# Performance work log

Measured on AMD Instinct MI355X. Metric: run time of the kernel, lower is better.

## Reference

```python
import jax, jax.numpy as jnp
import numpy as np

GROUPS = 8

def conv1d(x, w, b, stride=1, groups=1):
    # x: [B,C,L], w: [O, I//groups, K]
    y = jax.lax.conv_general_dilated(x, w, (stride,), 'VALID',
        dimension_numbers=('NCH', 'OIH', 'NCH'), feature_group_count=groups)
    return y + b[None, :, None]

def shuffle1d(x, groups):
    B, C, L = x.shape
    cpg = C // groups
    return x.reshape(B, groups, cpg, L).transpose(0, 2, 1, 3).reshape(B, C, L)

def setup_inputs() -> dict:
    key = jax.random.key(0)
    ks = jax.random.split(key, 12)
    C = 256
    B, L = 8, 4096
    g = GROUPS
    sc = 0.05
    inp = {
        'x':   jax.random.normal(ks[0], (B, C, L), dtype=jnp.float32),
        'w1':  jax.random.normal(ks[1], (C, C // g, 3), dtype=jnp.float32) * sc,
        'b1':  jax.random.normal(ks[2], (C,), dtype=jnp.float32) * sc,
        'w2':  jax.random.normal(ks[3], (C, C // g, 3), dtype=jnp.float32) * sc,
        'b2':  jax.random.normal(ks[4], (C,), dtype=jnp.float32) * sc,
        'wa1': jax.random.normal(ks[5], (C, 2 * C // g, 1), dtype=jnp.float32) * sc,
        'ba1': jax.random.normal(ks[6], (C,), dtype=jnp.float32) * sc,
        'wa2': jax.random.normal(ks[7], (C, C // g, 1), dtype=jnp.float32) * sc,
        'ba2': jax.random.normal(ks[8], (C,), dtype=jnp.float32) * sc,
        'w3':  jax.random.normal(ks[9], (C, C // g, 5), dtype=jnp.float32) * sc,  # kernel_size-4=5
        'b3':  jax.random.normal(ks[10], (C,), dtype=jnp.float32) * sc,
    }
    return inp

def reference(x, w1, b1, w2, b2, wa1, ba1, wa2, ba2, w3, b3):
    g = GROUPS
    # in_state has length 0 at init, so cat is identity; L >= kernel_size.
    h = conv1d(x, w1, b1, stride=1, groups=g)      # [B,C,L-2]
    h = shuffle1d(h, g)
    h = conv1d(h, w2, b2, stride=1, groups=g)      # [B,C,L-4]
    h = shuffle1d(h, g)
    # SortAttn: stable ascending sort over channel dim
    sorted_h = jnp.sort(h, axis=1, stable=True)
    a = conv1d(jnp.concatenate((sorted_h, h), axis=1), wa1, ba1, stride=1, groups=g)
    a = shuffle1d(a, g)
    a = jax.nn.sigmoid(conv1d(a, wa2, ba2, stride=1, groups=g))
    h = h * a
    y = conv1d(h, w3, b3, stride=1, groups=g)      # [B,C,L-8]
    return y
```

## Files before the change

### kernel.cpp

```cpp
#include <hip/hip_runtime.h>
#include <math.h>

#define BB 8
#define CCH 256
#define LLEN 4096
#define L1V 4094
#define L2V 4092
#define L3V 4088
#define NCOL (BB * L2V)

__global__ void prep_kernel(const float* __restrict__ wa1, const float* __restrict__ wa2,
                            const float* __restrict__ w1, const float* __restrict__ w2,
                            const float* __restrict__ w3,
                            float* __restrict__ wt1T, float* __restrict__ wt2T,
                            float* __restrict__ w1T, float* __restrict__ w2T,
                            float* __restrict__ w3T) {
    int r = blockIdx.x;
    int o = threadIdx.x;
    if (r < 64) {
        wt1T[r * 256 + o] = wa1[o * 64 + r];
    } else if (r < 96) {
        wt2T[(r - 64) * 256 + o] = wa2[o * 32 + (r - 64)];
    } else if (r < 192) {
        w1T[(r - 96) * 256 + o] = w1[o * 96 + (r - 96)];
    } else if (r < 288) {
        w2T[(r - 192) * 256 + o] = w2[o * 96 + (r - 192)];
    } else {
        w3T[(r - 288) * 256 + o] = w3[o * 160 + (r - 288)];
    }
}

__global__ __launch_bounds__(256, 4) void conv1_kernel(const float* __restrict__ x,
                                                       const float* __restrict__ w1T,
                                                       const float* __restrict__ b1,
                                                       float* __restrict__ t1) {
    __shared__ float xs[9248];
    const int b = blockIdx.y;
    const int l0 = blockIdx.x * 32;
    const int t = threadIdx.x;

#pragma unroll
    for (int j = 0; j < 9; ++j) {
        int f = t + 256 * j;
        int row = f / 9;
        int q = f - row * 9;
        size_t rb = (size_t)(b * CCH + row) * LLEN;
        float4 v;
        int base = l0 + 4 * q;
        if (base + 3 < LLEN) {
            v = *(const float4*)(x + rb + base);
        } else {
            v.x = x[rb + min(base + 0, LLEN - 1)];
            v.y = x[rb + min(base + 1, LLEN - 1)];
            v.z = x[rb + min(base + 2, LLEN - 1)];
            v.w = x[rb + min(base + 3, LLEN - 1)];
        }
        int a = row * 36 + (row >> 5) * 4 + 4 * q;
        *(float4*)&xs[a] = v;
    }
    __syncthreads();

    const int oc = t;
    const int go = t >> 5;
    float acc[32];
#pragma unroll
    for (int l = 0; l < 32; ++l) acc[l] = 0.f;

    for (int i = 0; i < 32; ++i) {
        int row = go * 32 + i;
        int base = row * 36 + go * 4;
        float wv0 = w1T[(i * 3 + 0) * 256 + oc];
        float wv1 = w1T[(i * 3 + 1) * 256 + oc];
        float wv2 = w1T[(i * 3 + 2) * 256 + oc];
#pragma unroll
        for (int q = 0; q < 9; ++q) {
            float4 v = *(const float4*)&xs[base + 4 * q];
#pragma unroll
            for (int j = 0; j < 4; ++j) {
                int e = 4 * q + j;
                float xv = (&v.x)[j];
                if (e < 32) acc[e] += wv0 * xv;
                if (e >= 1 && e <= 32) acc[e - 1] += wv1 * xv;
                if (e >= 2 && e <= 33) acc[e - 2] += wv2 * xv;
            }
        }
    }
    float bias = b1[oc];
    int nc = (oc & 31) * 8 + (oc >> 5);
    float* dst = t1 + (size_t)(b * L1V + l0) * CCH + nc;
#pragma unroll
    for (int l = 0; l < 32; ++l) {
        if (l0 + l < L1V) dst[(size_t)l * CCH] = acc[l] + bias;
    }
}

__global__ __launch_bounds__(256, 4) void conv2_kernel(const float* __restrict__ t1,
                                                       const float* __restrict__ w2T,
                                                       const float* __restrict__ b2,
                                                       float* __restrict__ t2) {
    __shared__ float ts[9792];
    const int b = blockIdx.y;
    const int l0 = blockIdx.x * 32;
    const int t = threadIdx.x;

#pragma unroll
    for (int j = 0; j < 9; ++j) {
        int f = t + 256 * j;
        if (f < 2176) {
            int p = f >> 6;
            int c4 = (f & 63) * 4;
            int row = min(l0 + p, L1V - 1);
            float4 v = *(const float4*)(t1 + (size_t)(b * L1V + row) * CCH + c4);
            *(float4*)&ts[p * 288 + (c4 >> 5) * 36 + (c4 & 31)] = v;
        }
    }
    __syncthreads();

    const int oc = t;
    const int go = t >> 5;
    float acc[32];
#pragma unroll
    for (int l = 0; l < 32; ++l) acc[l] = 0.f;

    for (int i4 = 0; i4 < 8; ++i4) {
        float wv[12];
#pragma unroll
        for (int z = 0; z < 12; ++z) wv[z] = w2T[(i4 * 12 + z) * 256 + oc];
        int colbase = go * 36 + i4 * 4;
#pragma unroll
        for (int p = 0; p < 34; ++p) {
            float4 rv = *(const float4*)&ts[p * 288 + colbase];
#pragma unroll
            for (int cc = 0; cc < 4; ++cc) {
                float xv = (&rv.x)[cc];
#pragma unroll
                for (int k = 0; k < 3; ++k) {
                    int l = p - k;
                    if (l >= 0 && l < 32) acc[l] += wv[cc * 3 + k] * xv;
                }
            }
        }
    }
    float bias = b2[oc];
    int nc = (oc & 31) * 8 + (oc >> 5);
    float* dst = t2 + (size_t)(b * L2V + l0) * CCH + nc;
#pragma unroll
    for (int l = 0; l < 32; ++l) {
        if (l0 + l < L2V) dst[(size_t)l * CCH] = acc[l] + bias;
    }
}

__device__ __forceinline__ void ce_pair(float& a, float& b, bool up) {
    float lo = fminf(a, b), hi = fmaxf(a, b);
    a = up ? lo : hi;
    b = up ? hi : lo;
}

template<int LM>
__device__ __forceinline__ float swz(float x) {
    return __int_as_float(__builtin_amdgcn_ds_swizzle(__float_as_int(x), (LM << 10) | 0x1F));
}

template<int K, int J>
__device__ __forceinline__ void mstep(float v[4][4], int lane) {
    if constexpr (J >= 4) {
        constexpr int LM = J >> 2;
        const bool upper = (lane & LM) != 0;
#pragma unroll
        for (int r = 0; r < 4; ++r) {
            const bool dirUp = (((4 * lane + r) & K) == 0);
            const bool keepMin = (dirUp != upper);
#pragma unroll
            for (int c = 0; c < 4; ++c) {
                float other;
                if constexpr (LM == 32) other = __shfl_xor(v[c][r], 32, 64);
                else other = swz<LM>(v[c][r]);
                float lo = fminf(v[c][r], other), hi = fmaxf(v[c][r], other);
                v[c][r] = keepMin ? lo : hi;
            }
        }
    } else if constexpr (J == 2) {
#pragma unroll
        for (int r = 0; r < 2; ++r) {
            const bool up = (((4 * lane + r) & K) == 0);
#pragma unroll
            for (int c = 0; c < 4; ++c) ce_pair(v[c][r], v[c][r + 2], up);
        }
    } else {
#pragma unroll
        for (int r = 0; r < 4; r += 2) {
            const bool up = (((4 * lane + r) & K) == 0);
#pragma unroll
            for (int c = 0; c < 4; ++c) ce_pair(v[c][r], v[c][r + 1], up);
        }
    }
    if constexpr (J > 1) mstep<K, (J >> 1)>(v, lane);
}

template<int K>
__device__ __forceinline__ void msort(float v[4][4], int lane) {
    mstep<K, (K >> 1)>(v, lane);
    if constexpr (K < 256) msort<(K << 1)>(v, lane);
}

__global__ __launch_bounds__(256, 5) void attn_kernel(float* __restrict__ t2,
                                                      const float* __restrict__ wt1T,
                                                      const float* __restrict__ wt2T,
                                                      const float* __restrict__ ba1,
                                                      const float* __restrict__ ba2) {
    __shared__ float sm[8192];
    const int t = threadIdx.x;
    const int wv = t >> 6;
    const int lane = t & 63;
    const int wbase = wv << 11;
    const int go = lane >> 3;

    float4 ba1v = *(const float4*)&ba1[4 * lane];
    float4 ba2v = *(const float4*)&ba2[4 * lane];

    const int colBase = blockIdx.x * 16 + wv * 4;

    float4 hv[4];
#pragma unroll
    for (int cc = 0; cc < 4; ++cc) {
        hv[cc] = *(const float4*)(t2 + (size_t)(colBase + cc) * CCH + 4 * lane);
    }
#pragma unroll
    for (int r = 0; r < 4; ++r) {
        int e = 4 * lane + r;
        int ch = (e >> 6) + 4;
        int slot = ch * 64 + ((e & 63) ^ ch);
        float4 vvv = make_float4((&hv[0].x)[r], (&hv[1].x)[r], (&hv[2].x)[r], (&hv[3].x)[r]);
        *(float4*)&sm[wbase + slot * 4] = vvv;
    }
    float v[4][4];
#pragma unroll
    for (int cc = 0; cc < 4; ++cc)
#pragma unroll
        for (int r = 0; r < 4; ++r) v[cc][r] = (&hv[cc].x)[r];
    msort<2>(v, lane);

#pragma unroll
    for (int r = 0; r < 4; ++r) {
        int e = 4 * lane + r;
        int ch = e >> 6;
        int slot = ch * 64 + ((e & 63) ^ ch);
        float4 vvv = make_float4(v[0][r], v[1][r], v[2][r], v[3][r]);
        *(float4*)&sm[wbase + slot * 4] = vvv;
    }

    float4 acc[4];
#pragma unroll
    for (int cc = 0; cc < 4; ++cc) acc[cc] = make_float4(0.f, 0.f, 0.f, 0.f);
#pragma unroll 4
    for (int i = 0; i < 64; ++i) {
        float4 w4 = *(const float4*)&wt1T[i * 256 + 4 * lane];
        float4 cv = *(const float4*)&sm[wbase + (go * 64 + (i ^ go)) * 4];
#pragma unroll
        for (int cc = 0; cc < 4; ++cc) {
            float cvv = (&cv.x)[cc];
            acc[cc].x += w4.x * cvv;
            acc[cc].y += w4.y * cvv;
            acc[cc].z += w4.z * cvv;
            acc[cc].w += w4.w * cvv;
        }
    }
#pragma unroll
    for (int r = 0; r < 4; ++r) {
        float bb = (&ba1v.x)[r];
        float4 vvv = make_float4((&acc[0].x)[r] + bb, (&acc[1].x)[r] + bb,
                                 (&acc[2].x)[r] + bb, (&acc[3].x)[r] + bb);
        *(float4*)&sm[wbase + (5 * lane + r) * 4] = vvv;
    }

    float4 acc2[4];
#pragma unroll
    for (int cc = 0; cc < 4; ++cc) acc2[cc] = make_float4(0.f, 0.f, 0.f, 0.f);
#pragma unroll 4
    for (int i = 0; i < 32; ++i) {
        float4 w4 = *(const float4*)&wt2T[i * 256 + 4 * lane];
        int idx = ((i & 7) << 5) + (go << 2) + (i >> 3);
        int slotA = idx + (idx >> 2);
        float4 av = *(const float4*)&sm[wbase + slotA * 4];
#pragma unroll
        for (int cc = 0; cc < 4; ++cc) {
            float avv = (&av.x)[cc];
            acc2[cc].x += w4.x * avv;
            acc2[cc].y += w4.y * avv;
            acc2[cc].z += w4.z * avv;
            acc2[cc].w += w4.w * avv;
        }
    }
#pragma unroll
    for (int cc = 0; cc < 4; ++cc) {
        float zx = acc2[cc].x + ba2v.x;
        float zy = acc2[cc].y + ba2v.y;
        float zz = acc2[cc].z + ba2v.z;
        float zw = acc2[cc].w + ba2v.w;
        float4 res;
        res.x = hv[cc].x * (1.f / (1.f + __expf(-zx)));
        res.y = hv[cc].y * (1.f / (1.f + __expf(-zy)));
        res.z = hv[cc].z * (1.f / (1.f + __expf(-zz)));
        res.w = hv[cc].w * (1.f / (1.f + __expf(-zw)));
        *(float4*)(t2 + (size_t)(colBase + cc) * CCH + 4 * lane) = res;
    }
}

__global__ __launch_bounds__(256, 4) void conv3_kernel(const float* __restrict__ hm,
                                                       const float* __restrict__ w3T,
                                                       const float* __restrict__ b3,
                                                       float* __restrict__ out) {
    __shared__ float ts[9216];
    const int b = blockIdx.y;
    const int l0 = blockIdx.x * 32;
    const int t = threadIdx.x;

#pragma unroll
    for (int j = 0; j < 9; ++j) {
        int f = t + 256 * j;
        int p = f >> 6;
        int c4 = (f & 63) * 4;
        int row = min(l0 + p, L2V - 1);
        float4 v = *(const float4*)(hm + (size_t)(b * L2V + row) * CCH + c4);
        *(float4*)&ts[p * 256 + c4] = v;
    }
    __syncthreads();

    const int oc = t;
    const int go = t >> 5;
    float acc[32];
#pragma unroll
    for (int l = 0; l < 32; ++l) acc[l] = 0.f;

    for (int i4 = 0; i4 < 8; ++i4) {
        float wv[20];
#pragma unroll
        for (int z = 0; z < 20; ++z) wv[z] = w3T[(i4 * 20 + z) * 256 + oc];
        int colbase = go * 32 + i4 * 4;
#pragma unroll
        for (int p = 0; p < 36; ++p) {
            float4 rv = *(const float4*)&ts[p * 256 + colbase];
#pragma unroll
            for (int cc = 0; cc < 4; ++cc) {
                float xv = (&rv.x)[cc];
#pragma unroll
                for (int k = 0; k < 5; ++k) {
                    int l = p - k;
                    if (l >= 0 && l < 32) acc[l] += wv[cc * 5 + k] * xv;
                }
            }
        }
    }
    float bias = b3[oc];
    float* dst = out + (size_t)(b * CCH + oc) * L3V + l0;
#pragma unroll
    for (int l4 = 0; l4 < 8; ++l4) {
        int gl = l0 + 4 * l4;
        if (gl + 3 < L3V) {
            float4 v;
            v.x = acc[4 * l4 + 0] + bias;
            v.y = acc[4 * l4 + 1] + bias;
            v.z = acc[4 * l4 + 2] + bias;
            v.w = acc[4 * l4 + 3] + bias;
            *(float4*)(dst + 4 * l4) = v;
        } else {
#pragma unroll
            for (int c = 0; c < 4; ++c) {
                if (gl + c < L3V) dst[4 * l4 + c] = acc[4 * l4 + c] + bias;
            }
        }
    }
}

extern "C" void kernel_launch(void* const* d_in, const int* in_sizes, int n_in,
                              void* d_out, int out_size, void* d_ws, size_t ws_size,
                              hipStream_t stream) {
    const float* x   = (const float*)d_in[0];
    const float* w1  = (const float*)d_in[1];
    const float* b1  = (const float*)d_in[2];
    const float* w2  = (const float*)d_in[3];
    const float* b2  = (const float*)d_in[4];
    const float* wa1 = (const float*)d_in[5];
    const float* ba1 = (const float*)d_in[6];
    const float* wa2 = (const float*)d_in[7];
    const float* ba2 = (const float*)d_in[8];
    const float* w3  = (const float*)d_in[9];
    const float* b3  = (const float*)d_in[10];
    float* out = (float*)d_out;

    char* ws = (char*)d_ws;
    float* t1   = (float*)ws;
    float* t2   = (float*)(ws + ((size_t)32 << 20));
    float* wt1T = (float*)(ws + ((size_t)64 << 20));
    float* wt2T = wt1T + 64 * 256;
    float* w1T  = wt2T + 32 * 256;
    float* w2T  = w1T + 96 * 256;
    float* w3T  = w2T + 96 * 256;

    hipLaunchKernelGGL(prep_kernel, dim3(448), dim3(256), 0, stream,
                       wa1, wa2, w1, w2, w3, wt1T, wt2T, w1T, w2T, w3T);
    hipLaunchKernelGGL(conv1_kernel, dim3(128, BB), dim3(256), 0, stream, x, w1T, b1, t1);
    hipLaunchKernelGGL(conv2_kernel, dim3(128, BB), dim3(256), 0, stream, t1, w2T, b2, t2);
    hipLaunchKernelGGL(attn_kernel, dim3(2046), dim3(256), 0, stream, t2, wt1T, wt2T, ba1, ba2);
    hipLaunchKernelGGL(conv3_kernel, dim3(128, BB), dim3(256), 0, stream, t2, w3T, b3, out);
}
```

Before: 284.5 us.

## Fuse conv1 and conv2 into one kernel with halo recompute in shared memory

Merges the first two grouped convolutions into a single kernel. Each block computes 34 conv1 output positions (a 2-column halo), writes them with the channel shuffle applied into shared memory, and then runs conv2 directly from shared memory. This removes the t1 global write and read round trip and one kernel launch. The cost is a small amount of recomputed halo work, 34 live accumulators instead of 32 (more register pressure), and an extra sync.

```diff
diff --git a/kernel.cpp b/kernel.cpp
--- a/kernel.cpp
+++ b/kernel.cpp
@@ -30,11 +30,13 @@
     }
 }
 
-__global__ __launch_bounds__(256, 4) void conv1_kernel(const float* __restrict__ x,
-                                                       const float* __restrict__ w1T,
-                                                       const float* __restrict__ b1,
-                                                       float* __restrict__ t1) {
-    __shared__ float xs[9248];
+__global__ __launch_bounds__(256, 4) void conv12_kernel(const float* __restrict__ x,
+                                                        const float* __restrict__ w1T,
+                                                        const float* __restrict__ b1,
+                                                        const float* __restrict__ w2T,
+                                                        const float* __restrict__ b2,
+                                                        float* __restrict__ t2) {
+    __shared__ float sm[9792];
     const int b = blockIdx.y;
     const int l0 = blockIdx.x * 32;
     const int t = threadIdx.x;
@@ -56,15 +58,16 @@
             v.w = x[rb + min(base + 3, LLEN - 1)];
         }
         int a = row * 36 + (row >> 5) * 4 + 4 * q;
-        *(float4*)&xs[a] = v;
+        *(float4*)&sm[a] = v;
     }
     __syncthreads();
 
     const int oc = t;
     const int go = t >> 5;
-    float acc[32];
-#pragma unroll
-    for (int l = 0; l < 32; ++l) acc[l] = 0.f;
+
+    float acc[34];
+#pragma unroll
+    for (int l = 0; l < 34; ++l) acc[l] = 0.f;
 
     for (int i = 0; i < 32; ++i) {
         int row = go * 32 + i;
@@ -74,53 +77,29 @@
         float wv2 = w1T[(i * 3 + 2) * 256 + oc];
 #pragma unroll
         for (int q = 0; q < 9; ++q) {
-            float4 v = *(const float4*)&xs[base + 4 * q];
+            float4 v = *(const float4*)&sm[base + 4 * q];
 #pragma unroll
             for (int j = 0; j < 4; ++j) {
                 int e = 4 * q + j;
                 float xv = (&v.x)[j];
-                if (e < 32) acc[e] += wv0 * xv;
-                if (e >= 1 && e <= 32) acc[e - 1] += wv1 * xv;
-                if (e >= 2 && e <= 33) acc[e - 2] += wv2 * xv;
-            }
-        }
-    }
-    float bias = b1[oc];
-    int nc = (oc & 31) * 8 + (oc >> 5);
-    float* dst = t1 + (size_t)(b * L1V + l0) * CCH + nc;
-#pragma unroll
-    for (int l = 0; l < 32; ++l) {
-        if (l0 + l < L1V) dst[(size_t)l * CCH] = acc[l] + bias;
-    }
-}
-
-__global__ __launch_bounds__(256, 4) void conv2_kernel(const float* __restrict__ t1,
-                                                       const float* __restrict__ w2T,
-                                                       const float* __restrict__ b2,
-                                                       float* __restrict__ t2) {
-    __shared__ float ts[9792];
-    const int b = blockIdx.y;
-    const int l0 = blockIdx.x * 32;
-    const int t = threadIdx.x;
-
-#pragma unroll
-    for (int j = 0; j < 9; ++j) {
-        int f = t + 256 * j;
-        if (f < 2176) {
-            int p = f >> 6;
-            int c4 = (f & 63) * 4;
-            int row = min(l0 + p, L1V - 1);
-            float4 v = *(const float4*)(t1 + (size_t)(b * L1V + row) * CCH + c4);
-            *(float4*)&ts[p * 288 + (c4 >> 5) * 36 + (c4 & 31)] = v;
-        }
-    }
+                if (e < 34) acc[e] += wv0 * xv;
+                if (e >= 1 && e <= 34) acc[e - 1] += wv1 * xv;
+                if (e >= 2) acc[e - 2] += wv2 * xv;
+            }
+        }
+    }
+    float bias1 = b1[oc];
+    int c1 = (oc & 31) * 8 + (oc >> 5);
+    int col1 = (c1 >> 5) * 36 + (c1 & 31);
+
     __syncthreads();
-
-    const int oc = t;
-    const int go = t >> 5;
-    float acc[32];
-#pragma unroll
-    for (int l = 0; l < 32; ++l) acc[l] = 0.f;
+#pragma unroll
+    for (int p = 0; p < 34; ++p) sm[p * 288 + col1] = acc[p] + bias1;
+    __syncthreads();
+
+    float acc2[32];
+#pragma unroll
+    for (int l = 0; l < 32; ++l) acc2[l] = 0.f;
 
     for (int i4 = 0; i4 < 8; ++i4) {
         float wv[12];
@@ -129,24 +108,24 @@
         int colbase = go * 36 + i4 * 4;
 #pragma unroll
         for (int p = 0; p < 34; ++p) {
-            float4 rv = *(const float4*)&ts[p * 288 + colbase];
+            float4 rv = *(const float4*)&sm[p * 288 + colbase];
 #pragma unroll
             for (int cc = 0; cc < 4; ++cc) {
                 float xv = (&rv.x)[cc];
 #pragma unroll
                 for (int k = 0; k < 3; ++k) {
                     int l = p - k;
-                    if (l >= 0 && l < 32) acc[l] += wv[cc * 3 + k] * xv;
+                    if (l >= 0 && l < 32) acc2[l] += wv[cc * 3 + k] * xv;
                 }
             }
         }
     }
-    float bias = b2[oc];
+    float bias2 = b2[oc];
     int nc = (oc & 31) * 8 + (oc >> 5);
     float* dst = t2 + (size_t)(b * L2V + l0) * CCH + nc;
 #pragma unroll
     for (int l = 0; l < 32; ++l) {
-        if (l0 + l < L2V) dst[(size_t)l * CCH] = acc[l] + bias;
+        if (l0 + l < L2V) dst[(size_t)l * CCH] = acc2[l] + bias2;
     }
 }
 
@@ -389,7 +368,6 @@
     float* out = (float*)d_out;
 
     char* ws = (char*)d_ws;
-    float* t1   = (float*)ws;
     float* t2   = (float*)(ws + ((size_t)32 << 20));
     float* wt1T = (float*)(ws + ((size_t)64 << 20));
     float* wt2T = wt1T + 64 * 256;
@@ -399,8 +377,8 @@
 
     hipLaunchKernelGGL(prep_kernel, dim3(448), dim3(256), 0, stream,
                        wa1, wa2, w1, w2, w3, wt1T, wt2T, w1T, w2T, w3T);
-    hipLaunchKernelGGL(conv1_kernel, dim3(128, BB), dim3(256), 0, stream, x, w1T, b1, t1);
-    hipLaunchKernelGGL(conv2_kernel, dim3(128, BB), dim3(256), 0, stream, t1, w2T, b2, t2);
+    hipLaunchKernelGGL(conv12_kernel, dim3(128, BB), dim3(256), 0, stream,
+                       x, w1T, b1, w2T, b2, t2);
     hipLaunchKernelGGL(attn_kernel, dim3(2046), dim3(256), 0, stream, t2, wt1T, wt2T, ba1, ba2);
     hipLaunchKernelGGL(conv3_kernel, dim3(128, BB), dim3(256), 0, stream, t2, w3T, b3, out);
 }
```

Result: slower. 531.1 us (+86.7%).
